# Performance work log

Measured on AMD Instinct MI355X. Metric: run time of the kernel, lower is better.

The kernel has to match this reference:

```python
import jax, jax.numpy as jnp
import numpy as np

DIM_LIST = [8, 8, 8, 8, 8, 8, 8, 8]
RANK_LIST = [1, 64, 64, 64, 64, 64, 64, 64, 1]
ORDER = 4                      # tensor_input_order
PADDED_IN = int(np.prod(DIM_LIST[:ORDER]))   # 4096
NUM_OUT = int(np.prod(DIM_LIST[ORDER:]))     # 4096
BATCH = 8192
NUM_IN = 4000                  # < PADDED_IN, exercises padding path


def setup_inputs() -> dict:
    key = jax.random.key(0)
    keys = jax.random.split(key, 10)
    x = jax.random.normal(keys[0], (BATCH, NUM_IN), dtype=jnp.float32)
    cores = {}
    for i in range(8):
        shp = (RANK_LIST[i], DIM_LIST[i], RANK_LIST[i + 1])
        cores[f"c{i}"] = 0.1 * jax.random.normal(keys[1 + i], shp, dtype=jnp.float32)
    bias = jax.random.normal(keys[9], (NUM_OUT,), dtype=jnp.float32)
    return {"x": x, **cores, "bias": bias}


def _tt_forward(x, cores, bias):
    B = x.shape[0]
    pad = PADDED_IN - x.shape[-1]
    xp = jnp.pad(x, ((0, 0), (0, pad))) if pad > 0 else x
    # ---- contract input modes with first ORDER cores ----
    z = xp.reshape(B, DIM_LIST[0], -1)            # (B, d0, M)
    z = jnp.einsum('bdm,dr->bmr', z, cores[0][0])  # core0 has r0=1
    for i in range(1, ORDER):
        d = DIM_LIST[i]
        Bz, M, r = z.shape
        z = z.reshape(B, d, M // d, r)
        z = jnp.einsum('bdmr,rds->bms', z, cores[i])
    # z: (B, 1, r_k)
    y = z
    # ---- expand output modes with remaining cores ----
    for i in range(ORDER, len(DIM_LIST)):
        y = jnp.einsum('bpr,rds->bpds', y, cores[i])
        y = y.reshape(B, -1, cores[i].shape[-1])
    out = y.reshape(B, -1)[:, :NUM_OUT]
    return out + bias


def reference(x, c0, c1, c2, c3, c4, c5, c6, c7, bias):
    cores = [c0, c1, c2, c3, c4, c5, c6, c7]
    return _tt_forward(x, cores, bias)
```

## Files before the change

kernel.cpp:

```cpp
#include <hip/hip_runtime.h>
#include <hip/hip_bf16.h>


typedef __attribute__((ext_vector_type(8))) short short8;
typedef __attribute__((ext_vector_type(4))) short s16x4;
typedef __attribute__((ext_vector_type(4))) float f32x4;

__device__ __forceinline__ short f2bf(float f) {
    union { float f; unsigned u; } c; c.f = f;
    unsigned u = c.u;
    unsigned r = (u + 0x7fffu + ((u >> 16) & 1u)) >> 16;
    return (short)r;
}

__global__ __launch_bounds__(64) void tt_heads(
    const float* __restrict__ c0, const float* __restrict__ c1,
    const float* __restrict__ c6, const float* __restrict__ c7,
    float* __restrict__ A2, float* __restrict__ B6) {
    const int t = threadIdx.x;
    if (blockIdx.x < 64) {
        const int b = blockIdx.x, i = b >> 3, d = b & 7;
        float acc = 0.f;
        for (int r = 0; r < 64; ++r)
            acc += c0[i * 64 + r] * c1[(r * 8 + d) * 64 + t];
        A2[b * 64 + t] = acc;
    } else {
        const int r = blockIdx.x - 64, d = t >> 3, j = t & 7;
        float acc = 0.f;
        for (int q = 0; q < 64; ++q)
            acc += c6[(r * 8 + d) * 64 + q] * c7[q * 8 + j];
        B6[r * 64 + t] = acc;
    }
}

__global__ __launch_bounds__(64) void tt_seconds(
    const float* __restrict__ A2, const float* __restrict__ c2,
    const float* __restrict__ B6, const float* __restrict__ c5,
    float* __restrict__ A3, float* __restrict__ B5) {
    const int t = threadIdx.x;
    if (blockIdx.x < 512) {
        const int row = blockIdx.x, i = row >> 3, d = row & 7;
        float acc = 0.f;
        for (int r = 0; r < 64; ++r)
            acc += A2[i * 64 + r] * c2[(r * 8 + d) * 64 + t];
        A3[row * 64 + t] = acc;
    } else {
        const int bb = blockIdx.x - 512, r = bb >> 3, d = bb & 7;
        float acc = 0.f;
        for (int q = 0; q < 64; ++q)
            acc += c5[(r * 8 + d) * 64 + q] * B6[q * 64 + t];
        B5[r * 512 + d * 64 + t] = acc;
    }
}

__global__ __launch_bounds__(256) void tt_chain_wide(
    const float* __restrict__ A3, const float* __restrict__ c3,
    const float* __restrict__ B5, const float* __restrict__ c4,
    short* __restrict__ A4f, short* __restrict__ B4t) {
    const int bid = blockIdx.x, t = threadIdx.x;
    if (bid < 1024) {
        const int k = (bid << 2) | (t >> 6);
        const int s = t & 63;
        const int i = k >> 3, d = k & 7;
        float acc = 0.f;
        for (int r = 0; r < 64; ++r)
            acc += A3[i * 64 + r] * c3[(r * 8 + d) * 64 + s];
        A4f[(((k >> 5) * 4 + (s >> 4)) << 9) + (((k >> 3) & 3) << 7) +
            ((s & 15) << 3) + (k & 7)] = f2bf(acc);
    } else {
        const int rd = bid - 1024;
        const int r = rd >> 3, d = rd & 7;
        for (int j = t; j < 512; j += 256) {
            float acc = 0.f;
            for (int q = 0; q < 64; ++q)
                acc += c4[(r * 8 + d) * 64 + q] * B5[q * 512 + j];
            B4t[(d * 512 + j) * 64 + r] = f2bf(acc);
        }
    }
}

__global__ __launch_bounds__(1024, 8) void gemm1_v2(
    const float* __restrict__ x, const short* __restrict__ A4f,
    short* __restrict__ zb) {
    __shared__ float zsm[16 * 1024];
    const int tid = threadIdx.x, wave = tid >> 6, lane = tid & 63;
    const int m0 = blockIdx.x << 4;
    const int r16 = lane & 15, hi = lane >> 4, kq = hi << 3;
    const float* xp = x + (long)(m0 + r16) * 4000 + kq;
    const short* a4p = A4f + (lane << 3);

    f32x4 acc[4] = {};
#pragma unroll 2
    for (int t = wave; t < 125; t += 16) {
        const int k0 = t << 5;
        f32x4 u0 = *(const f32x4*)(xp + k0);
        f32x4 u1 = *(const f32x4*)(xp + k0 + 4);
        short8 a;
        a[0] = f2bf(u0[0]); a[1] = f2bf(u0[1]);
        a[2] = f2bf(u0[2]); a[3] = f2bf(u0[3]);
        a[4] = f2bf(u1[0]); a[5] = f2bf(u1[1]);
        a[6] = f2bf(u1[2]); a[7] = f2bf(u1[3]);
#pragma unroll
        for (int f = 0; f < 4; ++f) {
            short8 b = *(const short8*)(a4p + (((t << 2) + f) << 9));
            acc[f] = __builtin_amdgcn_mfma_f32_16x16x32_bf16(a, b, acc[f], 0, 0, 0);
        }
    }
    const int prow = hi << 2;
#pragma unroll
    for (int f = 0; f < 4; ++f)
#pragma unroll
        for (int u = 0; u < 4; ++u)
            zsm[wave * 1024 + (prow + u) * 64 + f * 16 + r16] = acc[f][u];
    __syncthreads();
    if (tid < 256) {
        const f32x4* zp = (const f32x4*)zsm;
        f32x4 s = zp[tid];
#pragma unroll
        for (int w = 1; w < 16; ++w) s += zp[w * 256 + tid];
        s16x4 o;
#pragma unroll
        for (int u = 0; u < 4; ++u) o[u] = f2bf(s[u]);
        const int orow = tid >> 4, ocol = (tid & 15) << 2;
        *(s16x4*)(zb + (m0 + orow) * 64 + ocol) = o;
    }
}

#define BM 128
#define BN 128
#define BK 32

template <int K>
__global__ __launch_bounds__(256) void gemm_bias_kernel(
    const short* __restrict__ A,
    const short* __restrict__ Bt,
    const float* __restrict__ bias,
    float* __restrict__ C) {
    constexpr int N = 4096;
    __shared__ __align__(16) char smem[16384];
    short* As = (short*)smem;
    short* Bs = (short*)(smem + 8192);
    float* eps = (float*)smem;

    const int tid  = threadIdx.x;
    const int wave = tid >> 6;
    const int lane = tid & 63;

    const int bid = blockIdx.x;
    const int wg  = (bid & 7) * 256 + (bid >> 3);
    const int m0 = (wg >> 5) * BM;
    const int n0 = (wg & 31) * BN;

    const int c0i = tid;
    const int c1i = 256 + tid;
    const short* gA0 = A  + (m0 + (c0i >> 2)) * K + ((c0i & 3) << 3);
    const short* gA1 = A  + (m0 + (c1i >> 2)) * K + ((c1i & 3) << 3);
    const short* gB0 = Bt + (n0 + (c0i >> 2)) * K + ((c0i & 3) << 3);
    const short* gB1 = Bt + (n0 + (c1i >> 2)) * K + ((c1i & 3) << 3);
    short* lA0 = As + wave * 512;
    short* lA1 = As + 2048 + wave * 512;
    short* lB0 = Bs + wave * 512;
    short* lB1 = Bs + 2048 + wave * 512;

    const int wr = (wave >> 1) << 6;
    const int wc = (wave & 1) << 6;
    const int r16 = lane & 15;
    const int hi  = lane >> 4;
    const int kq  = hi << 3;

    f32x4 acc[4][4] = {};

    for (int kt = 0; kt < K / BK; ++kt) {
        __builtin_amdgcn_global_load_lds((const __attribute__((address_space(1))) void*)gA0,
                                         (__attribute__((address_space(3))) void*)lA0, 16, 0, 0);
        __builtin_amdgcn_global_load_lds((const __attribute__((address_space(1))) void*)gA1,
                                         (__attribute__((address_space(3))) void*)lA1, 16, 0, 0);
        __builtin_amdgcn_global_load_lds((const __attribute__((address_space(1))) void*)gB0,
                                         (__attribute__((address_space(3))) void*)lB0, 16, 0, 0);
        __builtin_amdgcn_global_load_lds((const __attribute__((address_space(1))) void*)gB1,
                                         (__attribute__((address_space(3))) void*)lB1, 16, 0, 0);
        gA0 += BK; gA1 += BK; gB0 += BK; gB1 += BK;
        __syncthreads();

        short8 a[4], b[4];
#pragma unroll
        for (int f = 0; f < 4; ++f) {
            a[f] = *(const short8*)(As + (wr + f * 16 + r16) * BK + kq);
            b[f] = *(const short8*)(Bs + (wc + f * 16 + r16) * BK + kq);
        }
#pragma unroll
        for (int i = 0; i < 4; ++i)
#pragma unroll
            for (int j = 0; j < 4; ++j)
                acc[i][j] = __builtin_amdgcn_mfma_f32_16x16x32_bf16(
                    a[i], b[j], acc[i][j], 0, 0, 0);
        __syncthreads();
    }

    float* slab = eps + wave * 1024;
    const f32x4 bzv = *(const f32x4*)(bias + n0 + wc + (r16 << 2));
#pragma unroll
    for (int i = 0; i < 4; ++i) {
        __syncthreads();
#pragma unroll
        for (int j = 0; j < 4; ++j)
#pragma unroll
            for (int u = 0; u < 4; ++u)
                slab[((hi << 2) + u) * 64 + j * 16 + r16] = acc[i][j][u];
        __syncthreads();
#pragma unroll
        for (int c = 0; c < 4; ++c) {
            const int lrow = (c << 2) + hi;
            f32x4 v = *(const f32x4*)(slab + lrow * 64 + (r16 << 2));
            v += bzv;
            const long row = m0 + wr + i * 16 + lrow;
            *(f32x4*)(C + row * N + n0 + wc + (r16 << 2)) = v;
        }
    }
}

extern "C" void kernel_launch(void* const* d_in, const int* in_sizes, int n_in,
                              void* d_out, int out_size, void* d_ws, size_t ws_size,
                              hipStream_t stream) {
    const float* x    = (const float*)d_in[0];
    const float* c0   = (const float*)d_in[1];
    const float* c1   = (const float*)d_in[2];
    const float* c2   = (const float*)d_in[3];
    const float* c3   = (const float*)d_in[4];
    const float* c4   = (const float*)d_in[5];
    const float* c5   = (const float*)d_in[6];
    const float* c6   = (const float*)d_in[7];
    const float* c7   = (const float*)d_in[8];
    const float* bias = (const float*)d_in[9];
    float* out = (float*)d_out;

    char* ws = (char*)d_ws;
    short* zb  = (short*)ws;
    short* A4f = (short*)(ws + (1u << 20));
    short* B4t = (short*)(ws + (1u << 20) + (512u << 10));
    float* A2  = (float*)(ws + (2u << 20));
    float* A3  = A2 + 64 * 64;
    float* B6  = A3 + 512 * 64;
    float* B5  = B6 + 64 * 64;

    tt_heads<<<128, 64, 0, stream>>>(c0, c1, c6, c7, A2, B6);
    tt_seconds<<<1024, 64, 0, stream>>>(A2, c2, B6, c5, A3, B5);
    tt_chain_wide<<<1536, 256, 0, stream>>>(A3, c3, B5, c4, A4f, B4t);

    gemm1_v2<<<512, 1024, 0, stream>>>(x, A4f, zb);
    gemm_bias_kernel<64><<<2048, 256, 0, stream>>>(zb, B4t, bias, out);
}
```

Measured before the change: 81.62 us.

## Fuse TT core-chain precompute into one kernel and use nontemporal x/output accesses

Merges the three small core-contraction kernels into a single kernel. Each block recomputes the intermediate rows it needs in shared memory instead of writing them to global memory between launches. This removes two kernel launches and their global round trips, at the cost of redundant recomputation of the A2/A3 and B6/B5 rows across blocks. It also switches the streaming x loads and output stores to nontemporal hints to reduce cache pollution.

```diff
diff --git a/kernel.cpp b/kernel.cpp
--- a/kernel.cpp
+++ b/kernel.cpp
@@ -13,68 +13,75 @@
     return (short)r;
 }
 
-__global__ __launch_bounds__(64) void tt_heads(
+__global__ __launch_bounds__(256) void tt_chain_fused(
     const float* __restrict__ c0, const float* __restrict__ c1,
+    const float* __restrict__ c2, const float* __restrict__ c3,
+    const float* __restrict__ c4, const float* __restrict__ c5,
     const float* __restrict__ c6, const float* __restrict__ c7,
-    float* __restrict__ A2, float* __restrict__ B6) {
+    short* __restrict__ A4f, short* __restrict__ B4t) {
+    __shared__ float sm[1024];
     const int t = threadIdx.x;
-    if (blockIdx.x < 64) {
-        const int b = blockIdx.x, i = b >> 3, d = b & 7;
-        float acc = 0.f;
-        for (int r = 0; r < 64; ++r)
-            acc += c0[i * 64 + r] * c1[(r * 8 + d) * 64 + t];
-        A2[b * 64 + t] = acc;
+    if (blockIdx.x < 1024) {
+        const int bid = blockIdx.x;
+        const int i = bid >> 1;
+        const int a2r = bid >> 4;
+        float* A2r_ = sm;
+        float* A3r_ = sm + 64;
+        if (t < 64) {
+            const int i1 = a2r >> 3, d1 = a2r & 7;
+            float acc = 0.f;
+            for (int r = 0; r < 64; ++r)
+                acc += c0[i1 * 64 + r] * c1[(r * 8 + d1) * 64 + t];
+            A2r_[t] = acc;
+        }
+        __syncthreads();
+        if (t < 64) {
+            const int d2 = i & 7;
+            float acc = 0.f;
+            for (int r = 0; r < 64; ++r)
+                acc += A2r_[r] * c2[(r * 8 + d2) * 64 + t];
+            A3r_[t] = acc;
+        }
+        __syncthreads();
+        {
+            const int kk = t >> 6, s = t & 63;
+            const int k = (bid << 2) + kk, d3 = k & 7;
+            float acc = 0.f;
+            for (int r = 0; r < 64; ++r)
+                acc += A3r_[r] * c3[(r * 8 + d3) * 64 + s];
+            A4f[(((k >> 5) * 4 + (s >> 4)) << 9) + (((k >> 3) & 3) << 7) +
+                ((s & 15) << 3) + (k & 7)] = f2bf(acc);
+        }
     } else {
-        const int r = blockIdx.x - 64, d = t >> 3, j = t & 7;
-        float acc = 0.f;
-        for (int q = 0; q < 64; ++q)
-            acc += c6[(r * 8 + d) * 64 + q] * c7[q * 8 + j];
-        B6[r * 64 + t] = acc;
-    }
-}
-
-__global__ __launch_bounds__(64) void tt_seconds(
-    const float* __restrict__ A2, const float* __restrict__ c2,
-    const float* __restrict__ B6, const float* __restrict__ c5,
-    float* __restrict__ A3, float* __restrict__ B5) {
-    const int t = threadIdx.x;
-    if (blockIdx.x < 512) {
-        const int row = blockIdx.x, i = row >> 3, d = row & 7;
-        float acc = 0.f;
-        for (int r = 0; r < 64; ++r)
-            acc += A2[i * 64 + r] * c2[(r * 8 + d) * 64 + t];
-        A3[row * 64 + t] = acc;
-    } else {
-        const int bb = blockIdx.x - 512, r = bb >> 3, d = bb & 7;
-        float acc = 0.f;
-        for (int q = 0; q < 64; ++q)
-            acc += c5[(r * 8 + d) * 64 + q] * B6[q * 64 + t];
-        B5[r * 512 + d * 64 + t] = acc;
-    }
-}
-
-__global__ __launch_bounds__(256) void tt_chain_wide(
-    const float* __restrict__ A3, const float* __restrict__ c3,
-    const float* __restrict__ B5, const float* __restrict__ c4,
-    short* __restrict__ A4f, short* __restrict__ B4t) {
-    const int bid = blockIdx.x, t = threadIdx.x;
-    if (bid < 1024) {
-        const int k = (bid << 2) | (t >> 6);
-        const int s = t & 63;
-        const int i = k >> 3, d = k & 7;
-        float acc = 0.f;
-        for (int r = 0; r < 64; ++r)
-            acc += A3[i * 64 + r] * c3[(r * 8 + d) * 64 + s];
-        A4f[(((k >> 5) * 4 + (s >> 4)) << 9) + (((k >> 3) & 3) << 7) +
-            ((s & 15) << 3) + (k & 7)] = f2bf(acc);
-    } else {
-        const int rd = bid - 1024;
-        const int r = rd >> 3, d = rd & 7;
-        for (int j = t; j < 512; j += 256) {
-            float acc = 0.f;
-            for (int q = 0; q < 64; ++q)
-                acc += c4[(r * 8 + d) * 64 + q] * B5[q * 512 + j];
-            B4t[(d * 512 + j) * 64 + r] = f2bf(acc);
+        const int cb = blockIdx.x - 1024;
+        const int d4 = cb & 7, jgrp = cb >> 3;
+        const int d5 = jgrp >> 3;
+        const int d6 = jgrp & 7;
+        float* B6l = sm;
+        float* B5l = sm + 512;
+        for (int o = t; o < 512; o += 256) {
+            const int q6 = o >> 3, jj = o & 7;
+            float acc = 0.f;
+            for (int q7 = 0; q7 < 64; ++q7)
+                acc += c6[(q6 * 8 + d6) * 64 + q7] * c7[q7 * 8 + jj];
+            B6l[o] = acc;
+        }
+        __syncthreads();
+        for (int o = t; o < 512; o += 256) {
+            const int q5 = o >> 3, jj = o & 7;
+            float acc = 0.f;
+            for (int q6 = 0; q6 < 64; ++q6)
+                acc += c5[(q5 * 8 + d5) * 64 + q6] * B6l[q6 * 8 + jj];
+            B5l[o] = acc;
+        }
+        __syncthreads();
+        for (int o = t; o < 512; o += 256) {
+            const int nl = o >> 6, r4 = o & 63;
+            float acc = 0.f;
+            for (int q5 = 0; q5 < 64; ++q5)
+                acc += c4[(r4 * 8 + d4) * 64 + q5] * B5l[q5 * 8 + nl];
+            const int n = d4 * 512 + jgrp * 8 + nl;
+            B4t[n * 64 + r4] = f2bf(acc);
         }
     }
 }
@@ -93,8 +100,8 @@
 #pragma unroll 2
     for (int t = wave; t < 125; t += 16) {
         const int k0 = t << 5;
-        f32x4 u0 = *(const f32x4*)(xp + k0);
-        f32x4 u1 = *(const f32x4*)(xp + k0 + 4);
+        f32x4 u0 = __builtin_nontemporal_load((const f32x4*)(xp + k0));
+        f32x4 u1 = __builtin_nontemporal_load((const f32x4*)(xp + k0 + 4));
         short8 a;
         a[0] = f2bf(u0[0]); a[1] = f2bf(u0[1]);
         a[2] = f2bf(u0[2]); a[3] = f2bf(u0[3]);
@@ -214,7 +221,7 @@
             f32x4 v = *(const f32x4*)(slab + lrow * 64 + (r16 << 2));
             v += bzv;
             const long row = m0 + wr + i * 16 + lrow;
-            *(f32x4*)(C + row * N + n0 + wc + (r16 << 2)) = v;
+            __builtin_nontemporal_store(v, (f32x4*)(C + row * N + n0 + wc + (r16 << 2)));
         }
     }
 }
@@ -238,15 +245,9 @@
     short* zb  = (short*)ws;
     short* A4f = (short*)(ws + (1u << 20));
     short* B4t = (short*)(ws + (1u << 20) + (512u << 10));
-    float* A2  = (float*)(ws + (2u << 20));
-    float* A3  = A2 + 64 * 64;
-    float* B6  = A3 + 512 * 64;
-    float* B5  = B6 + 64 * 64;
-
-    tt_heads<<<128, 64, 0, stream>>>(c0, c1, c6, c7, A2, B6);
-    tt_seconds<<<1024, 64, 0, stream>>>(A2, c2, B6, c5, A3, B5);
-    tt_chain_wide<<<1536, 256, 0, stream>>>(A3, c3, B5, c4, A4f, B4t);
-
+
+    tt_chain_fused<<<1536, 256, 0, stream>>>(c0, c1, c2, c3, c4, c5, c6, c7,
+                                             A4f, B4t);
     gemm1_v2<<<512, 1024, 0, stream>>>(x, A4f, zb);
     gemm_bias_kernel<64><<<2048, 256, 0, stream>>>(zb, B4t, bias, out);
 }
```

After: 87.02 us. 6.6% more time.
